# Kernel tuning notes

Hardware: AMD Instinct MI355X
Metric: run time of the kernel (lower is better)

The kernel has to match this reference:

```python
import jax, jax.numpy as jnp
import numpy as np

NUM_ITERATIONS = 3  # dynamic routing iterations
EPS = 1e-8
IN_LEN = 8   # capsule length after conv (out_length of CapsuleConv2d)
OUT_LEN = 16
OUT_CAPS = 10


def squash(s, axis=-1):
    # v = (|s|^2 / (1+|s|^2)) * s/|s|
    n2 = jnp.sum(s * s, axis=axis, keepdims=True)
    return (n2 / (1.0 + n2)) * s * jax.lax.rsqrt(n2 + EPS)


def setup_inputs() -> dict:
    key = jax.random.key(0)
    k1, k2, k3 = jax.random.split(key, 3)
    B = 16384
    x = jax.random.normal(k1, (B, 1, 3, 3), dtype=jnp.float32)
    # CapsuleConv2d weight: standard conv kernel [out_ch, in_ch, k, k]
    conv_w = 0.1 * jax.random.normal(k2, (32, 1, 3, 3), dtype=jnp.float32)
    # CapsuleLinear routing weight: [out_capsules, in_capsules, out_length, in_length]
    lin_w = 0.1 * jax.random.normal(k3, (OUT_CAPS, 36, OUT_LEN, IN_LEN), dtype=jnp.float32)
    return {"x": x, "conv_w": conv_w, "lin_w": lin_w}


def reference(x, conv_w, lin_w):
    B = x.shape[0]
    # --- CapsuleConv2d: conv2d (stride 1, pad 1) + squash over capsule length ---
    y = jax.lax.conv_general_dilated(
        x, conv_w, window_strides=(1, 1), padding=((1, 1), (1, 1)),
        dimension_numbers=("NCHW", "OIHW", "NCHW"))  # [B,32,3,3]
    H, W = y.shape[2], y.shape[3]
    G = y.shape[1] // IN_LEN  # 4 capsule groups of 8 channels
    y = y.reshape(B, G, IN_LEN, H, W)
    y = squash(y, axis=2)
    # capsules per spatial location: [B, H*W*G, in_length] = [B,36,8]
    caps = y.transpose(0, 3, 4, 1, 2).reshape(B, H * W * G, IN_LEN)

    # --- CapsuleLinear: priors + dynamic routing by agreement ---
    # priors[b,o,i,d] = sum_l lin_w[o,i,d,l] * caps[b,i,l]
    priors = jnp.einsum("oidl,bil->boid", lin_w, caps)  # [B,10,36,16]
    logits = jnp.zeros(priors.shape[:3] + (1,), dtype=priors.dtype)  # [B,10,36,1]
    out = None
    for it in range(NUM_ITERATIONS):
        probs = jax.nn.softmax(logits, axis=1)            # coupling over out_capsules
        out = squash(jnp.sum(probs * priors, axis=2))      # [B,10,16]
        if it != NUM_ITERATIONS - 1:
            # agreement: priors . out
            logits = logits + jnp.sum(priors * out[:, :, None, :], axis=-1, keepdims=True)
    return out  # [B,10,16]
```

## Files before the change

### kernel.cpp

```cpp
#include <hip/hip_runtime.h>

constexpr int OC = 10, NI = 36, OD = 16, IL = 8;
constexpr int M_BLK   = 16;
constexpr int M_INNER = 2;
constexpr int NGROUPS = M_BLK / M_INNER;
constexpr int NT      = 768;
constexpr int SROW    = 18;
constexpr int SPL_SZ  = OC * NI * SROW;

__global__ __launch_bounds__(NT, 1)
void capsnet_kernel(const float* __restrict__ xg,
                    const float* __restrict__ cwg,
                    const float* __restrict__ lwg,
                    float* __restrict__ outg) {
    __shared__ float xs[M_BLK * 9];
    __shared__ float cw[288];
    __shared__ float caps_t[IL * M_BLK * NI];
    __shared__ float spl[M_INNER * SPL_SZ];
    __shared__ float el[M_INNER * NI * OC];
    __shared__ float sinv[M_INNER * NI];
    __shared__ float outl[M_INNER * OC * OD];

    const int t  = threadIdx.x;
    const int b0 = blockIdx.x * M_BLK;

    if (t < M_BLK * 9) xs[t] = xg[b0 * 9 + t];
    if (t < 288)       cw[t] = cwg[t];

    const bool act = t < 2 * OC * NI;
    const int o  = t / (2 * NI);
    const int i  = (t % (2 * NI)) >> 1;
    const int dh = t & 1;

    float4 w4[16];
    if (act) {
        const float4* wp = reinterpret_cast<const float4*>(
            lwg + ((o * NI + i) * OD + dh * 8) * IL);
        #pragma unroll
        for (int j = 0; j < 16; ++j) w4[j] = wp[j];
    }
    __syncthreads();

    for (int task = t; task < M_BLK * NI; task += NT) {
        const int m  = task / NI;
        const int ci = task % NI;
        const int cg = ci & 3;
        const int wx = (ci >> 2) % 3;
        const int hx = ci / 12;
        float acc[IL] = {0.f,0.f,0.f,0.f,0.f,0.f,0.f,0.f};
        #pragma unroll
        for (int kh = 0; kh < 3; ++kh) {
            const int xh = hx + kh - 1;
            if (xh < 0 || xh > 2) continue;
            #pragma unroll
            for (int kw = 0; kw < 3; ++kw) {
                const int xw = wx + kw - 1;
                if (xw < 0 || xw > 2) continue;
                const float xv = xs[m * 9 + xh * 3 + xw];
                #pragma unroll
                for (int l = 0; l < IL; ++l)
                    acc[l] += xv * cw[(cg * 8 + l) * 9 + kh * 3 + kw];
            }
        }
        float n2 = 0.f;
        #pragma unroll
        for (int l = 0; l < IL; ++l) n2 += acc[l] * acc[l];
        const float sc = n2 / (1.f + n2) * rsqrtf(n2 + 1e-8f);
        #pragma unroll
        for (int l = 0; l < IL; ++l)
            caps_t[l * (M_BLK * NI) + task] = acc[l] * sc;
    }
    __syncthreads();

    for (int grp = 0; grp < NGROUPS; ++grp) {
        float P[M_INNER][8];
        float lg[M_INNER];
        float p[M_INNER];
        float ee[M_INNER];
        if (act) {
            #pragma unroll
            for (int m = 0; m < M_INNER; ++m) {
                float cc[IL];
                #pragma unroll
                for (int l = 0; l < IL; ++l)
                    cc[l] = caps_t[l * (M_BLK * NI) + (grp * M_INNER + m) * NI + i];
                #pragma unroll
                for (int d = 0; d < 8; ++d) {
                    const float4 a  = w4[d * 2];
                    const float4 b4 = w4[d * 2 + 1];
                    P[m][d] = a.x  * cc[0] + a.y  * cc[1] + a.z  * cc[2] + a.w  * cc[3]
                            + b4.x * cc[4] + b4.y * cc[5] + b4.z * cc[6] + b4.w * cc[7];
                }
                lg[m] = 0.f;
            }
        }
        p[0] = 0.1f; p[1] = 0.1f;

        for (int it = 0; it < 3; ++it) {
            if (act) {
                #pragma unroll
                for (int m = 0; m < M_INNER; ++m) {
                    float* row = &spl[m * SPL_SZ + (o * NI + i) * SROW + dh * 8];
                    #pragma unroll
                    for (int d = 0; d < 8; d += 2) {
                        float2 v = make_float2(p[m] * P[m][d], p[m] * P[m][d + 1]);
                        *reinterpret_cast<float2*>(row + d) = v;
                    }
                }
            }
            __syncthreads();
            if (t < M_INNER * OC * OD) {
                const int m  = t / (OC * OD);
                const int od = t % (OC * OD);
                const int oo = od / OD;
                const int d  = od % OD;
                const float* col = &spl[m * SPL_SZ + oo * NI * SROW + d];
                float s = 0.f;
                #pragma unroll
                for (int ii = 0; ii < NI; ++ii) s += col[ii * SROW];
                float n2 = s * s;
                n2 += __shfl_xor(n2, 1, 16);
                n2 += __shfl_xor(n2, 2, 16);
                n2 += __shfl_xor(n2, 4, 16);
                n2 += __shfl_xor(n2, 8, 16);
                const float sc = n2 / (1.f + n2) * rsqrtf(n2 + 1e-8f);
                const float ov = s * sc;
                if (it == 2) outg[(b0 + grp * M_INNER + m) * (OC * OD) + od] = ov;
                else         outl[m * (OC * OD) + od] = ov;
            }
            __syncthreads();
            if (it == 2) break;
            if (act) {
                #pragma unroll
                for (int m = 0; m < M_INNER; ++m) {
                    const float* om = &outl[m * (OC * OD) + o * OD + dh * 8];
                    float dpart = 0.f;
                    #pragma unroll
                    for (int d = 0; d < 8; ++d) dpart += P[m][d] * om[d];
                    const float delta = dpart + __shfl_xor(dpart, 1);
                    lg[m] += delta;
                    ee[m] = __expf(lg[m]);
                    if (dh == 0) el[m * (NI * OC) + i * OC + o] = ee[m];
                }
            }
            __syncthreads();
            if (t < M_INNER * NI) {
                const float* er = &el[(t / NI) * (NI * OC) + (t % NI) * OC];
                float ss = 0.f;
                #pragma unroll
                for (int o2 = 0; o2 < OC; ++o2) ss += er[o2];
                sinv[t] = 1.f / ss;
            }
            __syncthreads();
            if (act) {
                p[0] = ee[0] * sinv[i];
                p[1] = ee[1] * sinv[NI + i];
            }
        }
    }
}

extern "C" void kernel_launch(void* const* d_in, const int* in_sizes, int n_in,
                              void* d_out, int out_size, void* d_ws, size_t ws_size,
                              hipStream_t stream) {
    const float* x  = (const float*)d_in[0];
    const float* cw = (const float*)d_in[1];
    const float* lw = (const float*)d_in[2];
    float* out = (float*)d_out;
    const int B = in_sizes[0] / 9;
    dim3 grid(B / M_BLK), block(NT);
    capsnet_kernel<<<grid, block, 0, stream>>>(x, cw, lw, out);
}
```

Measured before the change: 225.3 us.

## Remap routing to one wavefront per output capsule with shuffle reductions

Restructures the routing so each 64-lane wavefront handles one output capsule: lanes cover 16 output dims by 4 input-capsule groups and hold priors for 4 samples in registers. Sums over input capsules and the squash norms become wave shuffles instead of shared-memory scatter and gather passes. The first iteration's uniform 0.1 coupling is applied directly, and the softmax state is kept as exp values in shared memory, cutting the number of barriers. Blocks shrink to 4 samples with 640 threads to raise occupancy. In exchange, routing weights are now read from global/L2 per block instead of being held in registers across 16 samples, and the per-prior agreement dot products need more shuffle traffic.

New measurement: 586.9 us. 161% more time.

```diff
diff --git a/kernel.cpp b/kernel.cpp
--- a/kernel.cpp
+++ b/kernel.cpp
@@ -1,53 +1,36 @@
 #include <hip/hip_runtime.h>
 
+
 constexpr int OC = 10, NI = 36, OD = 16, IL = 8;
-constexpr int M_BLK   = 16;
-constexpr int M_INNER = 2;
-constexpr int NGROUPS = M_BLK / M_INNER;
-constexpr int NT      = 768;
-constexpr int SROW    = 18;
-constexpr int SPL_SZ  = OC * NI * SROW;
+constexpr int M  = 4;
+constexpr int NT = 64 * OC;
 
-__global__ __launch_bounds__(NT, 1)
+__global__ __launch_bounds__(NT, 5)
 void capsnet_kernel(const float* __restrict__ xg,
                     const float* __restrict__ cwg,
                     const float* __restrict__ lwg,
-                    float* __restrict__ outg) {
-    __shared__ float xs[M_BLK * 9];
+                    float* __restrict__ outg)
+{
+    __shared__ float xs[M * 9];
     __shared__ float cw[288];
-    __shared__ float caps_t[IL * M_BLK * NI];
-    __shared__ float spl[M_INNER * SPL_SZ];
-    __shared__ float el[M_INNER * NI * OC];
-    __shared__ float sinv[M_INNER * NI];
-    __shared__ float outl[M_INNER * OC * OD];
+    __shared__ float caps[M * NI * IL];
+    __shared__ float pl[M * OC * NI];
+    __shared__ float sv[M * NI];
 
     const int t  = threadIdx.x;
-    const int b0 = blockIdx.x * M_BLK;
+    const int b0 = blockIdx.x * M;
 
-    if (t < M_BLK * 9) xs[t] = xg[b0 * 9 + t];
-    if (t < 288)       cw[t] = cwg[t];
-
-    const bool act = t < 2 * OC * NI;
-    const int o  = t / (2 * NI);
-    const int i  = (t % (2 * NI)) >> 1;
-    const int dh = t & 1;
-
-    float4 w4[16];
-    if (act) {
-        const float4* wp = reinterpret_cast<const float4*>(
-            lwg + ((o * NI + i) * OD + dh * 8) * IL);
-        #pragma unroll
-        for (int j = 0; j < 16; ++j) w4[j] = wp[j];
-    }
+    if (t < M * 9) xs[t] = xg[b0 * 9 + t];
+    if (t < 288)   cw[t] = cwg[t];
     __syncthreads();
 
-    for (int task = t; task < M_BLK * NI; task += NT) {
-        const int m  = task / NI;
-        const int ci = task % NI;
+    if (t < M * NI) {
+        const int m  = t / NI;
+        const int ci = t % NI;
         const int cg = ci & 3;
         const int wx = (ci >> 2) % 3;
         const int hx = ci / 12;
-        float acc[IL] = {0.f,0.f,0.f,0.f,0.f,0.f,0.f,0.f};
+        float acc[IL] = {};
         #pragma unroll
         for (int kh = 0; kh < 3; ++kh) {
             const int xh = hx + kh - 1;
@@ -67,96 +50,132 @@
         for (int l = 0; l < IL; ++l) n2 += acc[l] * acc[l];
         const float sc = n2 / (1.f + n2) * rsqrtf(n2 + 1e-8f);
         #pragma unroll
-        for (int l = 0; l < IL; ++l)
-            caps_t[l * (M_BLK * NI) + task] = acc[l] * sc;
+        for (int l = 0; l < IL; ++l) caps[t * IL + l] = acc[l] * sc;
     }
     __syncthreads();
 
-    for (int grp = 0; grp < NGROUPS; ++grp) {
-        float P[M_INNER][8];
-        float lg[M_INNER];
-        float p[M_INNER];
-        float ee[M_INNER];
-        if (act) {
-            #pragma unroll
-            for (int m = 0; m < M_INNER; ++m) {
-                float cc[IL];
-                #pragma unroll
-                for (int l = 0; l < IL; ++l)
-                    cc[l] = caps_t[l * (M_BLK * NI) + (grp * M_INNER + m) * NI + i];
-                #pragma unroll
-                for (int d = 0; d < 8; ++d) {
-                    const float4 a  = w4[d * 2];
-                    const float4 b4 = w4[d * 2 + 1];
-                    P[m][d] = a.x  * cc[0] + a.y  * cc[1] + a.z  * cc[2] + a.w  * cc[3]
-                            + b4.x * cc[4] + b4.y * cc[5] + b4.z * cc[6] + b4.w * cc[7];
-                }
-                lg[m] = 0.f;
+    const int o    = t >> 6;
+    const int lane = t & 63;
+    const int ig   = lane >> 4;
+    const int d    = lane & 15;
+
+    float P[M][9];
+    const float* wp = lwg + ((o * NI + ig) * OD + d) * IL;
+    #pragma unroll 3
+    for (int k = 0; k < 9; ++k) {
+        const float4 wa = *reinterpret_cast<const float4*>(wp + k * (4 * OD * IL));
+        const float4 wb = *reinterpret_cast<const float4*>(wp + k * (4 * OD * IL) + 4);
+        const int i = 4 * k + ig;
+        #pragma unroll
+        for (int m = 0; m < M; ++m) {
+            const float4 ca = *reinterpret_cast<const float4*>(&caps[(m * NI + i) * IL]);
+            const float4 cb = *reinterpret_cast<const float4*>(&caps[(m * NI + i) * IL + 4]);
+            P[m][k] = wa.x * ca.x + wa.y * ca.y + wa.z * ca.z + wa.w * ca.w
+                    + wb.x * cb.x + wb.y * cb.y + wb.z * cb.z + wb.w * cb.w;
+        }
+    }
+
+    float ov[M];
+
+    #pragma unroll
+    for (int m = 0; m < M; ++m) {
+        float s = 0.f;
+        #pragma unroll
+        for (int k = 0; k < 9; ++k) s += P[m][k];
+        s *= 0.1f;
+        s += __shfl_xor(s, 16);
+        s += __shfl_xor(s, 32);
+        float n2 = s * s;
+        n2 += __shfl_xor(n2, 1);
+        n2 += __shfl_xor(n2, 2);
+        n2 += __shfl_xor(n2, 4);
+        n2 += __shfl_xor(n2, 8);
+        const float sc = n2 / (1.f + n2) * rsqrtf(n2 + 1e-8f);
+        ov[m] = s * sc;
+    }
+    #pragma unroll
+    for (int m = 0; m < M; ++m) {
+        #pragma unroll
+        for (int k = 0; k < 9; ++k) {
+            float a = P[m][k] * ov[m];
+            a += __shfl_xor(a, 1);
+            a += __shfl_xor(a, 2);
+            a += __shfl_xor(a, 4);
+            a += __shfl_xor(a, 8);
+            if (d == 0) pl[(m * OC + o) * NI + 4 * k + ig] = __expf(a);
+        }
+    }
+    __syncthreads();
+    if (t < M * NI) {
+        const int m = t / NI, i = t % NI;
+        float ss = 0.f;
+        #pragma unroll
+        for (int oo = 0; oo < OC; ++oo) ss += pl[(m * OC + oo) * NI + i];
+        sv[t] = 1.f / ss;
+    }
+    __syncthreads();
+
+    #pragma unroll
+    for (int m = 0; m < M; ++m) {
+        float s = 0.f;
+        #pragma unroll
+        for (int k = 0; k < 9; ++k) {
+            const int i = 4 * k + ig;
+            s += pl[(m * OC + o) * NI + i] * sv[m * NI + i] * P[m][k];
+        }
+        s += __shfl_xor(s, 16);
+        s += __shfl_xor(s, 32);
+        float n2 = s * s;
+        n2 += __shfl_xor(n2, 1);
+        n2 += __shfl_xor(n2, 2);
+        n2 += __shfl_xor(n2, 4);
+        n2 += __shfl_xor(n2, 8);
+        const float sc = n2 / (1.f + n2) * rsqrtf(n2 + 1e-8f);
+        ov[m] = s * sc;
+    }
+    #pragma unroll
+    for (int m = 0; m < M; ++m) {
+        #pragma unroll
+        for (int k = 0; k < 9; ++k) {
+            float a = P[m][k] * ov[m];
+            a += __shfl_xor(a, 1);
+            a += __shfl_xor(a, 2);
+            a += __shfl_xor(a, 4);
+            a += __shfl_xor(a, 8);
+            if (d == 0) {
+                const int i   = 4 * k + ig;
+                const int idx = (m * OC + o) * NI + i;
+                pl[idx] = pl[idx] * sv[m * NI + i] * __expf(a);
             }
         }
-        p[0] = 0.1f; p[1] = 0.1f;
+    }
+    __syncthreads();
+    if (t < M * NI) {
+        const int m = t / NI, i = t % NI;
+        float ss = 0.f;
+        #pragma unroll
+        for (int oo = 0; oo < OC; ++oo) ss += pl[(m * OC + oo) * NI + i];
+        sv[t] = 1.f / ss;
+    }
+    __syncthreads();
 
-        for (int it = 0; it < 3; ++it) {
-            if (act) {
-                #pragma unroll
-                for (int m = 0; m < M_INNER; ++m) {
-                    float* row = &spl[m * SPL_SZ + (o * NI + i) * SROW + dh * 8];
-                    #pragma unroll
-                    for (int d = 0; d < 8; d += 2) {
-                        float2 v = make_float2(p[m] * P[m][d], p[m] * P[m][d + 1]);
-                        *reinterpret_cast<float2*>(row + d) = v;
-                    }
-                }
-            }
-            __syncthreads();
-            if (t < M_INNER * OC * OD) {
-                const int m  = t / (OC * OD);
-                const int od = t % (OC * OD);
-                const int oo = od / OD;
-                const int d  = od % OD;
-                const float* col = &spl[m * SPL_SZ + oo * NI * SROW + d];
-                float s = 0.f;
-                #pragma unroll
-                for (int ii = 0; ii < NI; ++ii) s += col[ii * SROW];
-                float n2 = s * s;
-                n2 += __shfl_xor(n2, 1, 16);
-                n2 += __shfl_xor(n2, 2, 16);
-                n2 += __shfl_xor(n2, 4, 16);
-                n2 += __shfl_xor(n2, 8, 16);
-                const float sc = n2 / (1.f + n2) * rsqrtf(n2 + 1e-8f);
-                const float ov = s * sc;
-                if (it == 2) outg[(b0 + grp * M_INNER + m) * (OC * OD) + od] = ov;
-                else         outl[m * (OC * OD) + od] = ov;
-            }
-            __syncthreads();
-            if (it == 2) break;
-            if (act) {
-                #pragma unroll
-                for (int m = 0; m < M_INNER; ++m) {
-                    const float* om = &outl[m * (OC * OD) + o * OD + dh * 8];
-                    float dpart = 0.f;
-                    #pragma unroll
-                    for (int d = 0; d < 8; ++d) dpart += P[m][d] * om[d];
-                    const float delta = dpart + __shfl_xor(dpart, 1);
-                    lg[m] += delta;
-                    ee[m] = __expf(lg[m]);
-                    if (dh == 0) el[m * (NI * OC) + i * OC + o] = ee[m];
-                }
-            }
-            __syncthreads();
-            if (t < M_INNER * NI) {
-                const float* er = &el[(t / NI) * (NI * OC) + (t % NI) * OC];
-                float ss = 0.f;
-                #pragma unroll
-                for (int o2 = 0; o2 < OC; ++o2) ss += er[o2];
-                sinv[t] = 1.f / ss;
-            }
-            __syncthreads();
-            if (act) {
-                p[0] = ee[0] * sinv[i];
-                p[1] = ee[1] * sinv[NI + i];
-            }
+    #pragma unroll
+    for (int m = 0; m < M; ++m) {
+        float s = 0.f;
+        #pragma unroll
+        for (int k = 0; k < 9; ++k) {
+            const int i = 4 * k + ig;
+            s += pl[(m * OC + o) * NI + i] * sv[m * NI + i] * P[m][k];
         }
+        s += __shfl_xor(s, 16);
+        s += __shfl_xor(s, 32);
+        float n2 = s * s;
+        n2 += __shfl_xor(n2, 1);
+        n2 += __shfl_xor(n2, 2);
+        n2 += __shfl_xor(n2, 4);
+        n2 += __shfl_xor(n2, 8);
+        const float sc = n2 / (1.f + n2) * rsqrtf(n2 + 1e-8f);
+        if (ig == 0) outg[(b0 + m) * (OC * OD) + o * OD + d] = s * sc;
     }
 }
 
@@ -164,10 +183,10 @@
                               void* d_out, int out_size, void* d_ws, size_t ws_size,
                               hipStream_t stream) {
     const float* x  = (const float*)d_in[0];
-    const float* cw = (const float*)d_in[1];
+    const float* cwp = (const float*)d_in[1];
     const float* lw = (const float*)d_in[2];
     float* out = (float*)d_out;
     const int B = in_sizes[0] / 9;
-    dim3 grid(B / M_BLK), block(NT);
-    capsnet_kernel<<<grid, block, 0, stream>>>(x, cw, lw, out);
+    dim3 grid(B / M), block(NT);
+    capsnet_kernel<<<grid, block, 0, stream>>>(x, cwp, lw, out);
 }
```
